# Performance work log

Measured on AMD Instinct MI355X. Metric: run time of the kernel, lower is better.

## Reference

```python
import jax, jax.numpy as jnp
import numpy as np
import math

B, S, D, H = 2, 2048, 1024, 16
DK = D // H


def setup_inputs() -> dict:
    key = jax.random.key(0)
    ks = jax.random.split(key, 8)
    s = 1.0 / math.sqrt(D)
    inp = {
        "query": jax.random.normal(ks[0], (B, S, D), jnp.float32),
        "key": jax.random.normal(ks[1], (B, S, D), jnp.float32),
        "value": jax.random.normal(ks[2], (B, S, D), jnp.float32),
        # causal mask: (1, 1, S, S), 1 where attention allowed
        "mask": jnp.tril(jnp.ones((S, S), jnp.int32))[None, None, :, :],
        "Wq": jax.random.normal(ks[3], (D, D), jnp.float32) * s,
        "Wk": jax.random.normal(ks[4], (D, D), jnp.float32) * s,
        "Wv": jax.random.normal(ks[5], (D, D), jnp.float32) * s,
        "Wo": jax.random.normal(ks[6], (D, D), jnp.float32) * s,
    }
    return inp


def reference(query, key, value, mask, Wq, Wk, Wv, Wo):
    # nn.Linear(bias=False): y = x @ W.T
    def proj_heads(x, W):
        y = jnp.einsum("bsd,ed->bse", x, W)          # (B,S,D)
        return y.reshape(B, -1, H, DK).transpose(0, 2, 1, 3)  # (B,H,S,DK)

    q = proj_heads(query, Wq)
    k = proj_heads(key, Wk)
    v = proj_heads(value, Wv)

    scale = jnp.asarray(math.sqrt(DK), q.dtype)
    scores = jnp.einsum("bhqd,bhkd->bhqk", q, k) / scale  # (B,H,S,S)
    scores = jnp.where(mask == 0, -jnp.inf, scores)
    attn = jax.nn.softmax(scores, axis=-1)
    # dropout p=0.0 (eval): identity
    out = jnp.einsum("bhqk,bhkd->bhqd", attn, v)          # (B,H,S,DK)
    concat = out.transpose(0, 2, 1, 3).reshape(B, -1, D)  # (B,S,D)
    return jnp.einsum("bsd,ed->bse", concat, Wo)
```

## Files before the change

kernel.cpp:

```cpp
#include <hip/hip_runtime.h>
#include <hip/hip_bf16.h>

#define B_ 2
#define S_ 2048
#define D_ 1024
#define H_ 16
#define DK_ 64

typedef __hip_bfloat16 bf16;
typedef __attribute__((ext_vector_type(8))) short bf16x8;
typedef __attribute__((ext_vector_type(4))) short bf16x4;
typedef __attribute__((ext_vector_type(4))) float f32x4;

#define GLDS16(g, l)                                                     \
    __builtin_amdgcn_global_load_lds(                                    \
        (const __attribute__((address_space(1))) void*)(g),              \
        (__attribute__((address_space(3))) void*)(l), 16, 0, 0)

#define MFMA_K32(a, b, c) __builtin_amdgcn_mfma_f32_16x16x32_bf16(a, b, c, 0, 0, 0)
#define MFMA_K16(a, b, c) __builtin_amdgcn_mfma_f32_16x16x16bf16_1k(a, b, c, 0, 0, 0)
#define EXP2F(x) __builtin_amdgcn_exp2f(x)

__global__ __launch_bounds__(256) void cvt_all(
    const float* __restrict__ q, const float* __restrict__ k, const float* __restrict__ v,
    const float* __restrict__ w0, const float* __restrict__ w1,
    const float* __restrict__ w2, const float* __restrict__ w3,
    bf16* __restrict__ oq, bf16* __restrict__ ok, bf16* __restrict__ ov,
    bf16* __restrict__ o0, bf16* __restrict__ o1, bf16* __restrict__ o2,
    bf16* __restrict__ o3) {
    int bid = blockIdx.x;
    const float* src; bf16* dst; int base;
    if      (bid < 2048) { src = q;  dst = oq; base = bid; }
    else if (bid < 4096) { src = k;  dst = ok; base = bid - 2048; }
    else if (bid < 6144) { src = v;  dst = ov; base = bid - 4096; }
    else if (bid < 6656) { src = w0; dst = o0; base = bid - 6144; }
    else if (bid < 7168) { src = w1; dst = o1; base = bid - 6656; }
    else if (bid < 7680) { src = w2; dst = o2; base = bid - 7168; }
    else                 { src = w3; dst = o3; base = bid - 7680; }
    int i = (base * 256 + threadIdx.x) * 8;
    float4 a = *(const float4*)(src + i);
    float4 b = *(const float4*)(src + i + 4);
    __align__(16) bf16 o[8];
    o[0] = __float2bfloat16(a.x); o[1] = __float2bfloat16(a.y);
    o[2] = __float2bfloat16(a.z); o[3] = __float2bfloat16(a.w);
    o[4] = __float2bfloat16(b.x); o[5] = __float2bfloat16(b.y);
    o[6] = __float2bfloat16(b.z); o[7] = __float2bfloat16(b.w);
    *(bf16x8*)(dst + i) = *(const bf16x8*)o;
}

__device__ __forceinline__ void proj_loop64(const bf16* __restrict__ X,
                                            const bf16* __restrict__ W,
                                            int m0, int n0, bf16* As, bf16* Bs,
                                            f32x4 (&acc)[2][4]) {
    const int K = D_;
    const int tid = threadIdx.x;
    const int lane = tid & 63, wave = tid >> 6;
    const int lm = lane & 15, quad = lane >> 4;

    auto stage = [&](int t, int bf) {
        int k0 = t * 64;
        bf16* Ab = As + bf * (128 * 64);
        bf16* Bb = Bs + bf * (64 * 64);
#pragma unroll
        for (int i = 0; i < 4; ++i) {
            int s = i * 256 + tid;
            int row = s >> 3, c = (s & 7) ^ (row & 7);
            GLDS16(X + (size_t)(m0 + row) * K + k0 + c * 8, Ab + s * 8);
        }
#pragma unroll
        for (int i = 0; i < 2; ++i) {
            int s = i * 256 + tid;
            int row = s >> 3, c = (s & 7) ^ (row & 7);
            GLDS16(W + (size_t)(n0 + row) * K + k0 + c * 8, Bb + s * 8);
        }
    };

    stage(0, 0);
    for (int t = 0; t < K / 64; ++t) {
        __syncthreads();
        if (t + 1 < K / 64) stage(t + 1, (t + 1) & 1);
        const bf16* Ab = As + (t & 1) * (128 * 64);
        const bf16* Bb = Bs + (t & 1) * (64 * 64);
#pragma unroll
        for (int ks = 0; ks < 2; ++ks) {
            bf16x8 aF[2], bF[4];
#pragma unroll
            for (int mt = 0; mt < 2; ++mt) {
                int row = wave * 32 + mt * 16 + lm;
                aF[mt] = *(const bf16x8*)(Ab + row * 64 +
                                          ((ks * 4 + quad) ^ (row & 7)) * 8);
            }
#pragma unroll
            for (int nt = 0; nt < 4; ++nt) {
                int row = nt * 16 + lm;
                bF[nt] = *(const bf16x8*)(Bb + row * 64 +
                                          ((ks * 4 + quad) ^ (row & 7)) * 8);
            }
#pragma unroll
            for (int mt = 0; mt < 2; ++mt)
#pragma unroll
                for (int nt = 0; nt < 4; ++nt)
                    acc[mt][nt] = MFMA_K32(aF[mt], bF[nt], acc[mt][nt]);
        }
    }
}

__global__ __launch_bounds__(256) void proj_qkv(
    const bf16* __restrict__ qx, const bf16* __restrict__ kx, const bf16* __restrict__ vx,
    const bf16* __restrict__ wq, const bf16* __restrict__ wk, const bf16* __restrict__ wv,
    bf16* __restrict__ qb, bf16* __restrict__ kb, bf16* __restrict__ vtb) {
    __shared__ __align__(16) bf16 As[2 * 128 * 64];
    __shared__ __align__(16) bf16 Bs[2 * 64 * 64];
    const int z = blockIdx.z;
    const bf16* X = (z == 0) ? qx : (z == 1) ? kx : vx;
    const bf16* W = (z == 0) ? wq : (z == 1) ? wk : wv;
    const int n0 = blockIdx.x * 64;
    const int m0 = blockIdx.y * 128;
    f32x4 acc[2][4] = {};
    proj_loop64(X, W, m0, n0, As, Bs, acc);

    const int lane = threadIdx.x & 63, wave = threadIdx.x >> 6;
    const int lm = lane & 15, quad = lane >> 4;
#pragma unroll
    for (int mt = 0; mt < 2; ++mt) {
        int mbase = m0 + wave * 32 + mt * 16 + quad * 4;
#pragma unroll
        for (int nt = 0; nt < 4; ++nt) {
            int n = n0 + nt * 16 + lm;
            if (z == 2) {
                int b = mbase >> 11, s = mbase & (S_ - 1);
                unsigned short u[4];
#pragma unroll
                for (int r = 0; r < 4; ++r) {
                    bf16 hv = __float2bfloat16(acc[mt][nt][r]);
                    u[r] = *(unsigned short*)&hv;
                }
                ushort4 pk = {u[0], u[1], u[2], u[3]};
                *(ushort4*)(vtb + ((size_t)(b * 1024 + n) * S_ + s)) = pk;
            } else {
                bf16* Y = z ? kb : qb;
#pragma unroll
                for (int r = 0; r < 4; ++r)
                    Y[(size_t)(mbase + r) * D_ + n] = __float2bfloat16(acc[mt][nt][r]);
            }
        }
    }
}

__global__ __launch_bounds__(256) void proj_o(const bf16* __restrict__ X,
                                              const bf16* __restrict__ W,
                                              float* __restrict__ Y) {
    __shared__ __align__(16) bf16 As[2 * 128 * 64];
    __shared__ __align__(16) bf16 Bs[2 * 64 * 64];
    const int n0 = blockIdx.x * 64;
    const int m0 = blockIdx.y * 128;
    f32x4 acc[2][4] = {};
    proj_loop64(X, W, m0, n0, As, Bs, acc);

    const int lane = threadIdx.x & 63, wave = threadIdx.x >> 6;
    const int lm = lane & 15, quad = lane >> 4;
#pragma unroll
    for (int mt = 0; mt < 2; ++mt) {
        int mbase = m0 + wave * 32 + mt * 16 + quad * 4;
#pragma unroll
        for (int nt = 0; nt < 4; ++nt) {
            int n = n0 + nt * 16 + lm;
#pragma unroll
            for (int r = 0; r < 4; ++r)
                Y[(size_t)(mbase + r) * D_ + n] = acc[mt][nt][r];
        }
    }
}

__global__ __launch_bounds__(512) void attn_kernel(const bf16* __restrict__ Q,
                                                   const bf16* __restrict__ Kb,
                                                   const bf16* __restrict__ VT,
                                                   bf16* __restrict__ O) {
    __shared__ __align__(16) bf16 kt[2][128 * 64];
    __shared__ __align__(16) bf16 vt[2][64 * 128];

    const int tid = threadIdx.x;
    const int lane = tid & 63, wave = tid >> 6;
    const int lm = lane & 15, quad = lane >> 4;
    const int f = (int)blockIdx.x;
    const int cls = f & 7;
    const int t = f >> 3;
    const int qi = 15 - (t >> 2);
    const int combo = cls + 8 * (t & 3);
    const int b = combo >> 4, h = combo & 15;
    const int q0 = qi * 128 + wave * 16;

    const size_t bhoff = (size_t)b * S_ * D_ + (size_t)h * DK_;
    const bf16* vtb = VT + ((size_t)b * 1024 + h * DK_) * S_;

    const bf16* qp = Q + bhoff + (size_t)(q0 + lm) * D_ + quad * 8;
    bf16x8 aq0 = *(const bf16x8*)(qp);
    bf16x8 aq1 = *(const bf16x8*)(qp + 32);

    f32x4 oacc[4] = {};
    float lsum = 0.f;
    const float cexp = 0.125f * 1.44269504f;

    auto stage = [&](int i, int bf) {
        int j0s = i * 128;
#pragma unroll
        for (int ii = 0; ii < 2; ++ii) {
            int s = ii * 512 + tid;
            int j = s >> 3, c = (s & 7) ^ (j & 7);
            GLDS16(Kb + bhoff + (size_t)(j0s + j) * D_ + c * 8, kt[bf] + s * 8);
        }
#pragma unroll
        for (int ii = 0; ii < 2; ++ii) {
            int s = ii * 512 + tid;
            int d = s >> 4, c = (s & 15) ^ (d & 15);
            GLDS16(vtb + (size_t)d * S_ + j0s + c * 8, vt[bf] + s * 8);
        }
    };

    auto chunk = [&](const bf16* ktb, const bf16* vtl, int st, bool mk) {
        int j = st * 16 + lm;
        bf16x8 bk0 = *(const bf16x8*)(ktb + (((j << 3) | (quad ^ (j & 7))) * 8));
        bf16x8 bk1 = *(const bf16x8*)(ktb + (((j << 3) | ((4 + quad) ^ (j & 7))) * 8));
        f32x4 z = {};
        z = MFMA_K32(bk0, aq0, z);
        z = MFMA_K32(bk1, aq1, z);
        bf16x4 pa;
        float rs = 0.f;
#pragma unroll
        for (int r = 0; r < 4; ++r) {
            float p = EXP2F(z[r] * cexp);
            if (mk && (quad * 4 + r > lm)) p = 0.f;
            rs += p;
            bf16 hv = __float2bfloat16(p);
            pa[r] = *(short*)&hv;
        }
        lsum += rs;
#pragma unroll
        for (int dt = 0; dt < 4; ++dt) {
            int d = dt * 16 + lm;
            int cl = st * 2 + (quad >> 1);
            bf16x4 bv = *(const bf16x4*)(vtl + d * 128 +
                                         ((cl ^ (d & 15)) * 8 + (quad & 1) * 4));
            oacc[dt] = MFMA_K16(pa, bv, oacc[dt]);
        }
    };

    stage(0, 0);

    for (int i = 0; i <= qi; ++i) {
        __syncthreads();
        if (i < qi) stage(i + 1, (i + 1) & 1);
        const bf16* ktb = kt[i & 1];
        const bf16* vtl = vt[i & 1];
        if (i < qi) {
#pragma unroll
            for (int st = 0; st < 8; ++st) chunk(ktb, vtl, st, false);
        } else {
            for (int st = 0; st < wave; ++st) chunk(ktb, vtl, st, false);
            chunk(ktb, vtl, wave, true);
        }
    }

    float l = lsum;
    l += __shfl_xor(l, 16, 64);
    l += __shfl_xor(l, 32, 64);
#pragma unroll
    for (int r = 0; r < 4; ++r) {
        float inv = 1.f / __shfl(l, quad * 4 + r, 64);
        int qrow = q0 + quad * 4 + r;
#pragma unroll
        for (int dt = 0; dt < 4; ++dt) {
            int d = dt * 16 + lm;
            O[bhoff + (size_t)qrow * D_ + d] = __float2bfloat16(oacc[dt][r] * inv);
        }
    }
}

extern "C" void kernel_launch(void* const* d_in, const int* in_sizes, int n_in,
                              void* d_out, int out_size, void* d_ws, size_t ws_size,
                              hipStream_t stream) {
    const float* q_in = (const float*)d_in[0];
    const float* k_in = (const float*)d_in[1];
    const float* v_in = (const float*)d_in[2];
    const float* Wq_f = (const float*)d_in[4];
    const float* Wk_f = (const float*)d_in[5];
    const float* Wv_f = (const float*)d_in[6];
    const float* Wo_f = (const float*)d_in[7];
    float* out = (float*)d_out;

    const size_t NEL = (size_t)B_ * S_ * D_;
    const size_t WEL = (size_t)D_ * D_;
    bf16* p = (bf16*)d_ws;
    bf16* qx = p;  p += NEL;
    bf16* kx = p;  p += NEL;
    bf16* vx = p;  p += NEL;
    bf16* wq = p;  p += WEL;
    bf16* wk = p;  p += WEL;
    bf16* wv = p;  p += WEL;
    bf16* wo = p;  p += WEL;
    bf16* qb = p;  p += NEL;
    bf16* kb = p;  p += NEL;
    bf16* vtb = p; p += NEL;
    bf16* cb = p;  p += NEL;

    cvt_all<<<8192, 256, 0, stream>>>(q_in, k_in, v_in, Wq_f, Wk_f, Wv_f, Wo_f,
                                      qx, kx, vx, wq, wk, wv, wo);

    dim3 gqkv(D_ / 64, (B_ * S_) / 128, 3);
    proj_qkv<<<gqkv, 256, 0, stream>>>(qx, kx, vx, wq, wk, wv, qb, kb, vtb);

    attn_kernel<<<dim3(512), 512, 0, stream>>>(qb, kb, vtb, cb);

    dim3 gproj(D_ / 64, (B_ * S_) / 128);
    proj_o<<<gproj, 256, 0, stream>>>(cb, wo, out);
}
```

Before: 219.7 us.

## Retile projection GEMMs to 128x128 output tiles with 32-wide K steps

Result: slower. 230.7 us (+5.0%).

```diff
diff --git a/kernel.cpp b/kernel.cpp
--- a/kernel.cpp
+++ b/kernel.cpp
@@ -48,60 +48,56 @@
     *(bf16x8*)(dst + i) = *(const bf16x8*)o;
 }
 
-__device__ __forceinline__ void proj_loop64(const bf16* __restrict__ X,
+__device__ __forceinline__ void proj_loop32(const bf16* __restrict__ X,
                                             const bf16* __restrict__ W,
                                             int m0, int n0, bf16* As, bf16* Bs,
-                                            f32x4 (&acc)[2][4]) {
+                                            f32x4 (&acc)[4][4]) {
     const int K = D_;
     const int tid = threadIdx.x;
     const int lane = tid & 63, wave = tid >> 6;
     const int lm = lane & 15, quad = lane >> 4;
+    const int wr = wave >> 1, wc = wave & 1;
 
     auto stage = [&](int t, int bf) {
-        int k0 = t * 64;
-        bf16* Ab = As + bf * (128 * 64);
-        bf16* Bb = Bs + bf * (64 * 64);
-#pragma unroll
-        for (int i = 0; i < 4; ++i) {
-            int s = i * 256 + tid;
-            int row = s >> 3, c = (s & 7) ^ (row & 7);
-            GLDS16(X + (size_t)(m0 + row) * K + k0 + c * 8, Ab + s * 8);
-        }
+        int k0 = t * 32;
+        bf16* Ab = As + bf * (128 * 32);
+        bf16* Bb = Bs + bf * (128 * 32);
 #pragma unroll
         for (int i = 0; i < 2; ++i) {
             int s = i * 256 + tid;
-            int row = s >> 3, c = (s & 7) ^ (row & 7);
+            int row = s >> 2, c = (s & 3) ^ (row & 3);
+            GLDS16(X + (size_t)(m0 + row) * K + k0 + c * 8, Ab + s * 8);
+        }
+#pragma unroll
+        for (int i = 0; i < 2; ++i) {
+            int s = i * 256 + tid;
+            int row = s >> 2, c = (s & 3) ^ (row & 3);
             GLDS16(W + (size_t)(n0 + row) * K + k0 + c * 8, Bb + s * 8);
         }
     };
 
     stage(0, 0);
-    for (int t = 0; t < K / 64; ++t) {
+    for (int t = 0; t < K / 32; ++t) {
         __syncthreads();
-        if (t + 1 < K / 64) stage(t + 1, (t + 1) & 1);
-        const bf16* Ab = As + (t & 1) * (128 * 64);
-        const bf16* Bb = Bs + (t & 1) * (64 * 64);
-#pragma unroll
-        for (int ks = 0; ks < 2; ++ks) {
-            bf16x8 aF[2], bF[4];
-#pragma unroll
-            for (int mt = 0; mt < 2; ++mt) {
-                int row = wave * 32 + mt * 16 + lm;
-                aF[mt] = *(const bf16x8*)(Ab + row * 64 +
-                                          ((ks * 4 + quad) ^ (row & 7)) * 8);
-            }
-#pragma unroll
-            for (int nt = 0; nt < 4; ++nt) {
-                int row = nt * 16 + lm;
-                bF[nt] = *(const bf16x8*)(Bb + row * 64 +
-                                          ((ks * 4 + quad) ^ (row & 7)) * 8);
-            }
-#pragma unroll
-            for (int mt = 0; mt < 2; ++mt)
-#pragma unroll
-                for (int nt = 0; nt < 4; ++nt)
-                    acc[mt][nt] = MFMA_K32(aF[mt], bF[nt], acc[mt][nt]);
-        }
+        if (t + 1 < K / 32) stage(t + 1, (t + 1) & 1);
+        const bf16* Ab = As + (t & 1) * (128 * 32);
+        const bf16* Bb = Bs + (t & 1) * (128 * 32);
+        bf16x8 aF[4], bF[4];
+#pragma unroll
+        for (int mt = 0; mt < 4; ++mt) {
+            int row = wr * 64 + mt * 16 + lm;
+            aF[mt] = *(const bf16x8*)(Ab + row * 32 + ((quad ^ (row & 3)) * 8));
+        }
+#pragma unroll
+        for (int nt = 0; nt < 4; ++nt) {
+            int row = wc * 64 + nt * 16 + lm;
+            bF[nt] = *(const bf16x8*)(Bb + row * 32 + ((quad ^ (row & 3)) * 8));
+        }
+#pragma unroll
+        for (int mt = 0; mt < 4; ++mt)
+#pragma unroll
+            for (int nt = 0; nt < 4; ++nt)
+                acc[mt][nt] = MFMA_K32(aF[mt], bF[nt], acc[mt][nt]);
     }
 }
 
@@ -109,24 +105,25 @@
     const bf16* __restrict__ qx, const bf16* __restrict__ kx, const bf16* __restrict__ vx,
     const bf16* __restrict__ wq, const bf16* __restrict__ wk, const bf16* __restrict__ wv,
     bf16* __restrict__ qb, bf16* __restrict__ kb, bf16* __restrict__ vtb) {
-    __shared__ __align__(16) bf16 As[2 * 128 * 64];
-    __shared__ __align__(16) bf16 Bs[2 * 64 * 64];
+    __shared__ __align__(16) bf16 As[2 * 128 * 32];
+    __shared__ __align__(16) bf16 Bs[2 * 128 * 32];
     const int z = blockIdx.z;
     const bf16* X = (z == 0) ? qx : (z == 1) ? kx : vx;
     const bf16* W = (z == 0) ? wq : (z == 1) ? wk : wv;
-    const int n0 = blockIdx.x * 64;
+    const int n0 = blockIdx.x * 128;
     const int m0 = blockIdx.y * 128;
-    f32x4 acc[2][4] = {};
-    proj_loop64(X, W, m0, n0, As, Bs, acc);
+    f32x4 acc[4][4] = {};
+    proj_loop32(X, W, m0, n0, As, Bs, acc);
 
     const int lane = threadIdx.x & 63, wave = threadIdx.x >> 6;
     const int lm = lane & 15, quad = lane >> 4;
-#pragma unroll
-    for (int mt = 0; mt < 2; ++mt) {
-        int mbase = m0 + wave * 32 + mt * 16 + quad * 4;
+    const int wr = wave >> 1, wc = wave & 1;
+#pragma unroll
+    for (int mt = 0; mt < 4; ++mt) {
+        int mbase = m0 + wr * 64 + mt * 16 + quad * 4;
 #pragma unroll
         for (int nt = 0; nt < 4; ++nt) {
-            int n = n0 + nt * 16 + lm;
+            int n = n0 + wc * 64 + nt * 16 + lm;
             if (z == 2) {
                 int b = mbase >> 11, s = mbase & (S_ - 1);
                 unsigned short u[4];
@@ -150,21 +147,22 @@
 __global__ __launch_bounds__(256) void proj_o(const bf16* __restrict__ X,
                                               const bf16* __restrict__ W,
                                               float* __restrict__ Y) {
-    __shared__ __align__(16) bf16 As[2 * 128 * 64];
-    __shared__ __align__(16) bf16 Bs[2 * 64 * 64];
-    const int n0 = blockIdx.x * 64;
+    __shared__ __align__(16) bf16 As[2 * 128 * 32];
+    __shared__ __align__(16) bf16 Bs[2 * 128 * 32];
+    const int n0 = blockIdx.x * 128;
     const int m0 = blockIdx.y * 128;
-    f32x4 acc[2][4] = {};
-    proj_loop64(X, W, m0, n0, As, Bs, acc);
+    f32x4 acc[4][4] = {};
+    proj_loop32(X, W, m0, n0, As, Bs, acc);
 
     const int lane = threadIdx.x & 63, wave = threadIdx.x >> 6;
     const int lm = lane & 15, quad = lane >> 4;
-#pragma unroll
-    for (int mt = 0; mt < 2; ++mt) {
-        int mbase = m0 + wave * 32 + mt * 16 + quad * 4;
+    const int wr = wave >> 1, wc = wave & 1;
+#pragma unroll
+    for (int mt = 0; mt < 4; ++mt) {
+        int mbase = m0 + wr * 64 + mt * 16 + quad * 4;
 #pragma unroll
         for (int nt = 0; nt < 4; ++nt) {
-            int n = n0 + nt * 16 + lm;
+            int n = n0 + wc * 64 + nt * 16 + lm;
 #pragma unroll
             for (int r = 0; r < 4; ++r)
                 Y[(size_t)(mbase + r) * D_ + n] = acc[mt][nt][r];
@@ -306,11 +304,11 @@
     cvt_all<<<8192, 256, 0, stream>>>(q_in, k_in, v_in, Wq_f, Wk_f, Wv_f, Wo_f,
                                       qx, kx, vx, wq, wk, wv, wo);
 
-    dim3 gqkv(D_ / 64, (B_ * S_) / 128, 3);
+    dim3 gqkv(D_ / 128, (B_ * S_) / 128, 3);
     proj_qkv<<<gqkv, 256, 0, stream>>>(qx, kx, vx, wq, wk, wv, qb, kb, vtb);
 
     attn_kernel<<<dim3(512), 512, 0, stream>>>(qb, kb, vtb, cb);
 
-    dim3 gproj(D_ / 64, (B_ * S_) / 128);
+    dim3 gproj(D_ / 128, (B_ * S_) / 128);
     proj_o<<<gproj, 256, 0, stream>>>(cb, wo, out);
 }
```
